# Kernel tuning notes

Hardware: AMD Instinct MI355X
Metric: run time of the kernel (lower is better)

## Reference

```python
import jax, jax.numpy as jnp
import numpy as np

EPS = 1e-5
HD = 16          # hidden_dim
OC = 256         # out_chs
NH = 8           # num_heads (groups of qkv conv)
DV = OC // (2 * HD)  # per-head value dim = 8


def conv_bn_silu(x, w, gamma, beta, mean, var, stride=1, pad=1, groups=1):
    # Conv2d(bias=False) + BatchNorm2d(eval) + SiLU, NCHW/OIHW
    y = jax.lax.conv_general_dilated(
        x, w, (stride, stride), [(pad, pad), (pad, pad)],
        dimension_numbers=('NCHW', 'OIHW', 'NCHW'),
        feature_group_count=groups)
    inv = gamma * jax.lax.rsqrt(var + EPS)
    y = y * inv[None, :, None, None] + (beta - mean * inv)[None, :, None, None]
    return y * jax.nn.sigmoid(y)


def _bn_params(key, c):
    k1, k2, k3, k4 = jax.random.split(key, 4)
    g = 1.0 + 0.1 * jax.random.normal(k1, (c,), jnp.float32)
    b = 0.1 * jax.random.normal(k2, (c,), jnp.float32)
    m = 0.1 * jax.random.normal(k3, (c,), jnp.float32)
    v = jax.random.uniform(k4, (c,), jnp.float32, 0.5, 1.5)
    return g, b, m, v


def setup_inputs() -> dict:
    key = jax.random.key(0)
    ks = jax.random.split(key, 8)
    B, C, H, W = 16, 256, 80, 80
    qkv_out = HD * 2 + OC // 2  # 160
    d = {}
    d['x'] = jax.random.normal(ks[0], (B, C, H, W), jnp.float32)
    # qkv_conv: grouped 3x3, groups=NH -> in per group = C//NH
    d['qkv_w'] = jax.random.normal(ks[1], (qkv_out, C // NH, 3, 3), jnp.float32) * 0.05
    d['qkv_g'], d['qkv_b'], d['qkv_m'], d['qkv_v'] = _bn_params(ks[2], qkv_out)
    # hidden_conv: dense 3x3
    d['hid_w'] = jax.random.normal(ks[3], (OC, C, 3, 3), jnp.float32) * 0.02
    d['hid_g'], d['hid_b'], d['hid_m'], d['hid_v'] = _bn_params(ks[4], OC)
    # out_conv: 1x1 on (OC//2*3) channels
    d['out_w'] = jax.random.normal(ks[5], (OC, OC // 2 * 3, 1, 1), jnp.float32) * 0.05
    d['out_g'], d['out_b'], d['out_m'], d['out_v'] = _bn_params(ks[6], OC)
    return d


def reference(x, qkv_w, qkv_g, qkv_b, qkv_m, qkv_v,
              hid_w, hid_g, hid_b, hid_m, hid_v,
              out_w, out_g, out_b, out_m, out_v):
    B, C, H, W = x.shape
    N = H * W
    qkv = conv_bn_silu(x, qkv_w, qkv_g, qkv_b, qkv_m, qkv_v, stride=1, pad=1, groups=NH)
    q = qkv[:, :HD]               # (B, HD, H, W)
    k = qkv[:, HD:2 * HD]
    v = qkv[:, 2 * HD:]           # (B, OC//2, H, W)
    # permute to (B, N, HD) / (B, N, HD, DV), channel-major reshape matches torch .view
    q = q.transpose(0, 2, 3, 1).reshape(B, N, HD)
    k = k.transpose(0, 2, 3, 1).reshape(B, N, HD)
    v = v.transpose(0, 2, 3, 1).reshape(B, N, HD, DV)
    # per-pixel tiny attention: attn[b,n,i,j] = softmax_j(q_i * k_j)
    attn = jax.nn.softmax(q[..., :, None] * k[..., None, :], axis=-1)  # (B,N,HD,HD)
    y = jnp.einsum('bnij,bnjd->bnid', attn, v)                          # (B,N,HD,DV)
    # torch: permute(0,2,3,1).view(B, OC//2, H, W)
    y = y.transpose(0, 2, 3, 1).reshape(B, OC // 2, H, W)
    h = conv_bn_silu(x, hid_w, hid_g, hid_b, hid_m, hid_v, stride=1, pad=1)
    y = jnp.concatenate([y, h], axis=1)  # (B, OC//2*3, H, W)
    return conv_bn_silu(y, out_w, out_g, out_b, out_m, out_v, stride=1, pad=0)
```

## Files before the change

kernel.cpp:

```cpp
#include <hip/hip_runtime.h>
#include <stdint.h>

typedef unsigned short u16;
typedef unsigned int u32;
typedef __attribute__((ext_vector_type(4))) float f32x4;
typedef __attribute__((ext_vector_type(8))) __bf16 bf16x8;

#define EPS_BN 1e-5f

__device__ __forceinline__ u16 f2bf(float f) {
  u32 u = __builtin_bit_cast(u32, f);
  u32 r = (u + 0x7fffu + ((u >> 16) & 1u)) >> 16;
  return (u16)r;
}

__device__ __forceinline__ float silu_f(float v) {
  return v / (1.0f + __expf(-v));
}

__device__ __forceinline__ void gll16(const void* g, void* l) {
  __builtin_amdgcn_global_load_lds(
      (__attribute__((address_space(1))) void*)(void*)g,
      (__attribute__((address_space(3))) void*)l, 16, 0, 0);
}

__global__ __launch_bounds__(256) void prep(
    const float* __restrict__ qkv_w, const float* __restrict__ qg,
    const float* __restrict__ qb, const float* __restrict__ qm,
    const float* __restrict__ qv,
    const float* __restrict__ hid_w, const float* __restrict__ hg,
    const float* __restrict__ hb, const float* __restrict__ hm,
    const float* __restrict__ hv,
    const float* __restrict__ out_w, const float* __restrict__ og,
    const float* __restrict__ ob, const float* __restrict__ om,
    const float* __restrict__ ov,
    u16* __restrict__ wtb, u16* __restrict__ w2b, u16* __restrict__ wqp,
    float* __restrict__ bnq_s, float* __restrict__ bnq_b,
    float* __restrict__ bnh_s, float* __restrict__ bnh_b,
    float* __restrict__ bn2s, float* __restrict__ bn2b,
    float* __restrict__ zpg)
{
  const int gid = blockIdx.x * 256 + threadIdx.x;
  if (gid < 256 * 2304) {
    int j = gid / 2304, k = gid - j * 2304;
    int tap = k >> 8, c = k & 255;
    wtb[gid] = f2bf(hid_w[(j * 256 + c) * 9 + tap]);
  }
  if (gid < 73728) {
    int g = gid / 9216;
    int r = gid - g * 9216;
    int j = r / 288, k = r - j * 288;
    int tap = k >> 5, cg = k & 31;
    float v = 0.f;
    if (j < 20) v = qkv_w[((g * 20 + j) * 32 + cg) * 9 + tap];
    wqp[gid] = f2bf(v);
  }
  if (gid < 98304) w2b[gid] = f2bf(out_w[gid]);
  if (gid < 160) {
    float iv = qg[gid] * rsqrtf(qv[gid] + EPS_BN);
    bnq_s[gid] = iv; bnq_b[gid] = qb[gid] - qm[gid] * iv;
  }
  if (gid < 256) {
    float iv = hg[gid] * rsqrtf(hv[gid] + EPS_BN);
    bnh_s[gid] = iv; bnh_b[gid] = hb[gid] - hm[gid] * iv;
    float iv2 = og[gid] * rsqrtf(ov[gid] + EPS_BN);
    bn2s[gid] = iv2; bn2b[gid] = ob[gid] - om[gid] * iv2;
  }
  if (gid < 64) zpg[gid] = 0.f;
}

__global__ __launch_bounds__(256) void nchw2nhwc(
    const float* __restrict__ x, u16* __restrict__ xn)
{
  __shared__ u16 T[80 * 66];
  const int t = threadIdx.x;
  const int ct = blockIdx.x;
  const int h  = blockIdx.y;
  const int b  = blockIdx.z;
  const float* src = x + ((size_t)b * 256 + ct * 64) * 6400 + h * 80;
  for (int it = 0; it < 5; ++it) {
    int idx = it * 256 + t;
    int cl = idx / 20, w4 = idx - cl * 20;
    float4 v = *(const float4*)(src + (size_t)cl * 6400 + w4 * 4);
    T[(w4 * 4 + 0) * 66 + cl] = f2bf(v.x);
    T[(w4 * 4 + 1) * 66 + cl] = f2bf(v.y);
    T[(w4 * 4 + 2) * 66 + cl] = f2bf(v.z);
    T[(w4 * 4 + 3) * 66 + cl] = f2bf(v.w);
  }
  __syncthreads();
  u16* dst = xn + ((size_t)(b * 80 + h) * 80) * 256 + ct * 64;
  for (int it = 0; it < 5; ++it) {
    int idx = it * 256 + t;
    int wl = idx >> 4;
    int cl = (idx & 15) * 4;
    ushort4 v4;
    v4.x = T[wl * 66 + cl + 0];
    v4.y = T[wl * 66 + cl + 1];
    v4.z = T[wl * 66 + cl + 2];
    v4.w = T[wl * 66 + cl + 3];
    *(ushort4*)(dst + (size_t)wl * 256 + cl) = v4;
  }
}

__global__ __launch_bounds__(512, 4) void gemm_main(
    const u16* __restrict__ xn, const u16* __restrict__ wt,
    const float* __restrict__ bns, const float* __restrict__ bnb,
    const float* __restrict__ zpg, u16* __restrict__ ycat)
{
  __shared__ __attribute__((aligned(16))) u16 Al[128 * 64];
  __shared__ __attribute__((aligned(16))) u16 Bl[256 * 64];
  const int t = threadIdx.x;
  const int wave = t >> 6, lane = t & 63;
  const int wm = wave >> 2;
  const int wn = wave & 3;
  const int orig = blockIdx.x;
  const int wg = (orig & 7) * 100 + (orig >> 3);
  const int ptile = wg * 128;

  const int srcc = (((lane & 7) ^ ((lane >> 3) & 7)) * 8);
  const int c16 = lane & 15, lq = lane >> 4;

  int pbA[2], hhA[2], wwA[2];
#pragma unroll
  for (int l = 0; l < 2; ++l) {
    int row = wave * 8 + (lane >> 3) + l * 64;
    int p = ptile + row;
    pbA[l] = p;
    int hw = p % 6400;
    hhA[l] = hw / 80;
    wwA[l] = hw - (hw / 80) * 80;
  }
  int bofB[4];
#pragma unroll
  for (int l = 0; l < 4; ++l) {
    int row = wave * 8 + (lane >> 3) + l * 64;
    bofB[l] = row * 2304 + srcc;
  }

  f32x4 acc[4][4];
#pragma unroll
  for (int m = 0; m < 4; ++m)
#pragma unroll
    for (int n = 0; n < 4; ++n) {
      f32x4 z = {0.f, 0.f, 0.f, 0.f};
      acc[m][n] = z;
    }

  for (int ks = 0; ks < 36; ++ks) {
    const int k0 = ks * 64;
    const int tap = ks >> 2;
    const int c0 = (ks & 3) * 64;
    const int dh = tap / 3 - 1, dw = tap - (tap / 3) * 3 - 1;
    const int dp = dh * 80 + dw;
    __syncthreads();
#pragma unroll
    for (int l = 0; l < 2; ++l) {
      bool ok = ((unsigned)(hhA[l] + dh) < 80u) & ((unsigned)(wwA[l] + dw) < 80u);
      const u16* src = ok
          ? (xn + ((size_t)(pbA[l] + dp) * 256 + c0 + srcc))
          : (const u16*)zpg;
      gll16(src, Al + (wave * 8 + l * 64) * 64);
    }
#pragma unroll
    for (int l = 0; l < 4; ++l)
      gll16(wt + (size_t)(bofB[l] + k0), Bl + (wave * 8 + l * 64) * 64);
    __syncthreads();
#pragma unroll
    for (int kk = 0; kk < 2; ++kk) {
      const int q = kk * 4 + lq;
      bf16x8 av[4], bv[4];
#pragma unroll
      for (int m = 0; m < 4; ++m) {
        int r = wm * 64 + m * 16 + c16;
        av[m] = *(const bf16x8*)(Al + r * 64 + (q ^ (r & 7)) * 8);
      }
#pragma unroll
      for (int n = 0; n < 4; ++n) {
        int j = wn * 64 + n * 16 + c16;
        bv[n] = *(const bf16x8*)(Bl + j * 64 + (q ^ (j & 7)) * 8);
      }
#pragma unroll
      for (int m = 0; m < 4; ++m)
#pragma unroll
        for (int n = 0; n < 4; ++n)
          acc[m][n] = __builtin_amdgcn_mfma_f32_16x16x32_bf16(
              av[m], bv[n], acc[m][n], 0, 0, 0);
    }
  }

  const int rg = lq;
#pragma unroll
  for (int n = 0; n < 4; ++n) {
    int j = wn * 64 + n * 16 + c16;
    float sc = bns[j], bi = bnb[j];
#pragma unroll
    for (int m = 0; m < 4; ++m) {
      int p0 = ptile + wm * 64 + m * 16 + rg * 4;
#pragma unroll
      for (int r = 0; r < 4; ++r) {
        float v = silu_f(acc[m][n][r] * sc + bi);
        ycat[(size_t)(p0 + r) * 384 + 128 + j] = f2bf(v);
      }
    }
  }
}

__global__ __launch_bounds__(256, 2) void qkv_attn(
    const u16* __restrict__ xn, const u16* __restrict__ wqp,
    const float* __restrict__ bnq_s, const float* __restrict__ bnq_b,
    u16* __restrict__ ycat)
{
  __shared__ __attribute__((aligned(16))) char LB[81920];
  u16* HB0 = (u16*)LB;
  u16* HB1 = (u16*)(LB + 40960);
  float* qs = (float*)LB;

  const int t = threadIdx.x;
  const int wave = t >> 6, lane = t & 63;
  const int orig = blockIdx.x;
  const int wg = (orig & 7) * 100 + (orig >> 3);
  const int ptile = wg * 128;
  const int pbase = ptile - 88;

  const int srcc = (((lane & 7) ^ ((lane >> 3) & 7)) * 8);
  const int q = lane >> 4, c16 = lane & 15;

  int ph[2], pw[2];
#pragma unroll
  for (int m = 0; m < 2; ++m) {
    int p = ptile + wave * 32 + m * 16 + c16;
    int hw = p % 6400;
    ph[m] = hw / 80;
    pw[m] = hw - (hw / 80) * 80;
  }

  auto STAGE_H = [&](int cc, u16* dst) {
#pragma unroll
    for (int r = 0; r < 10; ++r) {
      int row = r * 32 + wave * 8 + (lane >> 3);
      int p = pbase + row;
      int pc = p < 0 ? 0 : (p > 102399 ? 102399 : p);
      gll16(xn + (size_t)pc * 256 + cc * 64 + srcc,
            dst + (r * 32 + wave * 8) * 64);
    }
  };

  bf16x8 zv;
#pragma unroll
  for (int i = 0; i < 8; ++i) zv[i] = (__bf16)0.0f;

  f32x4 acc[2][16];
#pragma unroll
  for (int m = 0; m < 2; ++m)
#pragma unroll
    for (int f = 0; f < 16; ++f) {
      f32x4 z = {0.f, 0.f, 0.f, 0.f};
      acc[m][f] = z;
    }

  STAGE_H(0, HB0);
  asm volatile("s_waitcnt vmcnt(0)" ::: "memory");
  __builtin_amdgcn_sched_barrier(0);
  __syncthreads();

#pragma unroll
  for (int cc = 0; cc < 4; ++cc) {
    const u16* HBc = (cc & 1) ? HB1 : HB0;
    u16* HBn = (cc & 1) ? HB0 : HB1;
    if (cc < 3) STAGE_H(cc + 1, HBn);
    for (int tap = 0; tap < 9; ++tap) {
      const int dh = tap / 3 - 1, dw = tap - (tap / 3) * 3 - 1;
      const int dp = dh * 80 + dw;
      bf16x8 bq[2][2];
#pragma unroll
      for (int h = 0; h < 2; ++h)
#pragma unroll
        for (int nf = 0; nf < 2; ++nf) {
          int row = (2 * cc + h) * 32 + nf * 16 + c16;
          bq[h][nf] =
              *(const bf16x8*)(wqp + (size_t)row * 288 + tap * 32 + q * 8);
        }
      bf16x8 av[2][2];
#pragma unroll
      for (int m = 0; m < 2; ++m) {
        int rl = wave * 32 + m * 16 + c16 + 88 + dp;
        bool ok = ((unsigned)(ph[m] + dh) < 80u) &
                  ((unsigned)(pw[m] + dw) < 80u);
#pragma unroll
        for (int h = 0; h < 2; ++h) {
          int q8 = h * 4 + q;
          bf16x8 raw = *(const bf16x8*)(HBc + rl * 64 + ((q8 ^ (rl & 7)) * 8));
          av[m][h] = ok ? raw : zv;
        }
      }
#pragma unroll
      for (int h = 0; h < 2; ++h)
#pragma unroll
        for (int m = 0; m < 2; ++m)
#pragma unroll
          for (int nf = 0; nf < 2; ++nf)
            acc[m][(2 * cc + h) * 2 + nf] = __builtin_amdgcn_mfma_f32_16x16x32_bf16(
                av[m][h], bq[h][nf], acc[m][(2 * cc + h) * 2 + nf], 0, 0, 0);
    }
    if (cc < 3) {
      asm volatile("s_waitcnt vmcnt(0)" ::: "memory");
      __builtin_amdgcn_sched_barrier(0);
      __syncthreads();
    }
  }

  asm volatile("s_waitcnt vmcnt(0)" ::: "memory");
  __builtin_amdgcn_sched_barrier(0);
  __syncthreads();

#pragma unroll
  for (int f = 0; f < 16; ++f) {
    int jj = (f & 1) * 16 + c16;
    if (jj >= 20) continue;
    int oc = (f >> 1) * 20 + jj;
    float sc = bnq_s[oc], bi = bnq_b[oc];
#pragma unroll
    for (int m = 0; m < 2; ++m) {
      int pl0 = wave * 32 + m * 16 + q * 4;
#pragma unroll
      for (int r = 0; r < 4; ++r)
        qs[(pl0 + r) * 160 + oc] = silu_f(acc[m][f][r] * sc + bi);
    }
  }
  __syncthreads();

  for (int it = 0; it < 8; ++it) {
    int idx = it * 256 + t;
    int px = idx >> 4, i = idx & 15;
    const float* row = qs + px * 160;
    const float qi = row[i];
    float s[16];
    float mx = -3.4e38f;
#pragma unroll
    for (int j = 0; j < 16; ++j) { s[j] = qi * row[16 + j]; mx = fmaxf(mx, s[j]); }
    float sum = 0.f;
#pragma unroll
    for (int j = 0; j < 16; ++j) { s[j] = __expf(s[j] - mx); sum += s[j]; }
    const float inv = 1.0f / sum;
    float y[8];
#pragma unroll
    for (int d = 0; d < 8; ++d) y[d] = 0.f;
#pragma unroll
    for (int j = 0; j < 16; ++j) {
      const float a = s[j];
      const float* vr = row + 32 + j * 8;
#pragma unroll
      for (int d = 0; d < 8; ++d) y[d] += a * vr[d];
    }
    union { u16 u[8]; uint4 v4; } pk;
#pragma unroll
    for (int d = 0; d < 8; ++d) pk.u[d] = f2bf(y[d] * inv);
    *(uint4*)(ycat + (size_t)(ptile + px) * 384 + i * 8) = pk.v4;
  }
}

__global__ __launch_bounds__(256, 2) void gemm_out(
    const u16* __restrict__ w2, const u16* __restrict__ ycat,
    const float* __restrict__ bns, const float* __restrict__ bnb,
    float* __restrict__ out)
{
  __shared__ __attribute__((aligned(16))) u16 Al[128 * 64];
  __shared__ __attribute__((aligned(16))) u16 Bl[128 * 64];
  const int t = threadIdx.x;
  const int wave = t >> 6, lane = t & 63;
  const int wr = wave >> 1, wc = wave & 1;
  const int orig = blockIdx.y * 2 + blockIdx.x;
  const int wg = (orig & 7) * 200 + (orig >> 3);
  const int octile = (wg / 800) * 128;
  const int ptile = (wg % 800) * 128;

  const int srcc = (((lane & 7) ^ ((lane >> 3) & 7)) * 8);
  int bofA[4], bofB[4];
#pragma unroll
  for (int c = 0; c < 4; ++c) {
    int m = wave * 32 + c * 8 + (lane >> 3);
    bofA[c] = (octile + m) * 384 + srcc;
    bofB[c] = (ptile + m) * 384 + srcc;
  }
  u16* AlW = Al + wave * 2048;
  u16* BlW = Bl + wave * 2048;

  f32x4 acc[4][4];
#pragma unroll
  for (int m = 0; m < 4; ++m)
#pragma unroll
    for (int n = 0; n < 4; ++n) {
      f32x4 z = {0.f, 0.f, 0.f, 0.f};
      acc[m][n] = z;
    }

  for (int ks = 0; ks < 6; ++ks) {
    const int k0 = ks * 64;
    __syncthreads();
#pragma unroll
    for (int c = 0; c < 4; ++c) gll16(w2 + (size_t)(bofA[c] + k0), AlW + c * 512);
#pragma unroll
    for (int c = 0; c < 4; ++c) gll16(ycat + (size_t)(bofB[c] + k0), BlW + c * 512);
    __syncthreads();
#pragma unroll
    for (int kk = 0; kk < 2; ++kk) {
      const int q = kk * 4 + (lane >> 4);
      const int c16 = lane & 15;
      bf16x8 av[4], bv[4];
#pragma unroll
      for (int m = 0; m < 4; ++m) {
        int r = wr * 64 + m * 16 + c16;
        av[m] = *(const bf16x8*)(Al + r * 64 + (q ^ (r & 7)) * 8);
      }
#pragma unroll
      for (int n = 0; n < 4; ++n) {
        int r = wc * 64 + n * 16 + c16;
        bv[n] = *(const bf16x8*)(Bl + r * 64 + (q ^ (r & 7)) * 8);
      }
#pragma unroll
      for (int m = 0; m < 4; ++m)
#pragma unroll
        for (int n = 0; n < 4; ++n)
          acc[m][n] = __builtin_amdgcn_mfma_f32_16x16x32_bf16(
              av[m], bv[n], acc[m][n], 0, 0, 0);
    }
  }

  const int c16 = lane & 15, rg = lane >> 4;
  const int b = ptile / 6400;
  const int hwb = ptile - b * 6400;
#pragma unroll
  for (int m = 0; m < 4; ++m) {
    int oc0 = octile + wr * 64 + m * 16 + rg * 4;
#pragma unroll
    for (int n = 0; n < 4; ++n) {
      int hw = hwb + wc * 64 + n * 16 + c16;
#pragma unroll
      for (int r = 0; r < 4; ++r) {
        int oc = oc0 + r;
        float v = silu_f(acc[m][n][r] * bns[oc] + bnb[oc]);
        out[((size_t)b * 256 + oc) * 6400 + hw] = v;
      }
    }
  }
}

extern "C" void kernel_launch(void* const* d_in, const int* in_sizes, int n_in,
                              void* d_out, int out_size, void* d_ws, size_t ws_size,
                              hipStream_t stream) {
  (void)in_sizes; (void)n_in; (void)out_size; (void)ws_size;
  const float* x    = (const float*)d_in[0];
  const float* qkvw = (const float*)d_in[1];
  const float* qg   = (const float*)d_in[2];
  const float* qb   = (const float*)d_in[3];
  const float* qm   = (const float*)d_in[4];
  const float* qv   = (const float*)d_in[5];
  const float* hw_  = (const float*)d_in[6];
  const float* hg   = (const float*)d_in[7];
  const float* hb   = (const float*)d_in[8];
  const float* hm   = (const float*)d_in[9];
  const float* hv   = (const float*)d_in[10];
  const float* ow   = (const float*)d_in[11];
  const float* og   = (const float*)d_in[12];
  const float* ob   = (const float*)d_in[13];
  const float* om   = (const float*)d_in[14];
  const float* ov   = (const float*)d_in[15];

  char* ws = (char*)d_ws;
  float* zpg   = (float*)(ws + 0);
  float* bnq_s = (float*)(ws + 256);
  float* bnq_b = (float*)(ws + 1280);
  float* bnh_s = (float*)(ws + 2304);
  float* bnh_b = (float*)(ws + 3328);
  float* bn2s  = (float*)(ws + 4352);
  float* bn2b  = (float*)(ws + 5376);
  u16*   wtb   = (u16*)(ws + 6400);
  u16*   w2b   = (u16*)(ws + 1186048);
  u16*   wqp   = (u16*)(ws + 1382656);
  u16*   xn    = (u16*)(ws + 1536000);
  u16*   ycat  = (u16*)(ws + 119500800);
  float* out   = (float*)d_out;

  prep<<<dim3(2304), dim3(256), 0, stream>>>(
      qkvw, qg, qb, qm, qv, hw_, hg, hb, hm, hv, ow, og, ob, om, ov,
      wtb, w2b, wqp, bnq_s, bnq_b, bnh_s, bnh_b, bn2s, bn2b, zpg);
  nchw2nhwc<<<dim3(4, 80, 16), dim3(256), 0, stream>>>(x, xn);
  gemm_main<<<dim3(800), dim3(512), 0, stream>>>(
      xn, wtb, bnh_s, bnh_b, zpg, ycat);
  qkv_attn<<<dim3(800), dim3(256), 0, stream>>>(
      xn, wqp, bnq_s, bnq_b, ycat);
  gemm_out<<<dim3(2, 800), dim3(256), 0, stream>>>(
      w2b, ycat, bn2s, bn2b, out);
}
```

Before: 302.4 us.

## Load input halo once per channel chunk and reuse across all 3x3 taps

The implicit-GEMM 3x3 conv now loads a 320-row halo of input pixels per 64-channel chunk into LDS once and reads shifted rows for each of the 9 taps, instead of reloading the A tile for every tap. Out-of-image taps are masked in registers with a zero vector, so the zero-page global pointer is no longer needed. This is meant to cut global/L2 traffic for the activation operand roughly ninefold. In exchange LDS use grows (320x64 A plus 256x64 B per block), which can reduce occupancy, and the swizzled reads at shifted rows may introduce bank conflicts.

```diff
diff --git a/kernel.cpp b/kernel.cpp
--- a/kernel.cpp
+++ b/kernel.cpp
@@ -105,9 +105,9 @@
 __global__ __launch_bounds__(512, 4) void gemm_main(
     const u16* __restrict__ xn, const u16* __restrict__ wt,
     const float* __restrict__ bns, const float* __restrict__ bnb,
-    const float* __restrict__ zpg, u16* __restrict__ ycat)
+    u16* __restrict__ ycat)
 {
-  __shared__ __attribute__((aligned(16))) u16 Al[128 * 64];
+  __shared__ __attribute__((aligned(16))) u16 HA[320 * 64];
   __shared__ __attribute__((aligned(16))) u16 Bl[256 * 64];
   const int t = threadIdx.x;
   const int wave = t >> 6, lane = t & 63;
@@ -116,26 +116,29 @@
   const int orig = blockIdx.x;
   const int wg = (orig & 7) * 100 + (orig >> 3);
   const int ptile = wg * 128;
+  const int pbase = ptile - 88;
 
   const int srcc = (((lane & 7) ^ ((lane >> 3) & 7)) * 8);
   const int c16 = lane & 15, lq = lane >> 4;
 
-  int pbA[2], hhA[2], wwA[2];
-#pragma unroll
-  for (int l = 0; l < 2; ++l) {
-    int row = wave * 8 + (lane >> 3) + l * 64;
-    int p = ptile + row;
-    pbA[l] = p;
+  int ph[4], pw[4];
+#pragma unroll
+  for (int m = 0; m < 4; ++m) {
+    int p = ptile + wm * 64 + m * 16 + c16;
     int hw = p % 6400;
-    hhA[l] = hw / 80;
-    wwA[l] = hw - (hw / 80) * 80;
+    ph[m] = hw / 80;
+    pw[m] = hw - (hw / 80) * 80;
   }
   int bofB[4];
 #pragma unroll
   for (int l = 0; l < 4; ++l) {
-    int row = wave * 8 + (lane >> 3) + l * 64;
+    int row = l * 64 + wave * 8 + (lane >> 3);
     bofB[l] = row * 2304 + srcc;
   }
+
+  bf16x8 zv;
+#pragma unroll
+  for (int i = 0; i < 8; ++i) zv[i] = (__bf16)0.0f;
 
   f32x4 acc[4][4];
 #pragma unroll
@@ -146,45 +149,52 @@
       acc[m][n] = z;
     }
 
-  for (int ks = 0; ks < 36; ++ks) {
-    const int k0 = ks * 64;
-    const int tap = ks >> 2;
-    const int c0 = (ks & 3) * 64;
-    const int dh = tap / 3 - 1, dw = tap - (tap / 3) * 3 - 1;
-    const int dp = dh * 80 + dw;
+#pragma unroll
+  for (int cc = 0; cc < 4; ++cc) {
+    const int c0 = cc * 64;
     __syncthreads();
 #pragma unroll
-    for (int l = 0; l < 2; ++l) {
-      bool ok = ((unsigned)(hhA[l] + dh) < 80u) & ((unsigned)(wwA[l] + dw) < 80u);
-      const u16* src = ok
-          ? (xn + ((size_t)(pbA[l] + dp) * 256 + c0 + srcc))
-          : (const u16*)zpg;
-      gll16(src, Al + (wave * 8 + l * 64) * 64);
-    }
-#pragma unroll
-    for (int l = 0; l < 4; ++l)
-      gll16(wt + (size_t)(bofB[l] + k0), Bl + (wave * 8 + l * 64) * 64);
-    __syncthreads();
-#pragma unroll
-    for (int kk = 0; kk < 2; ++kk) {
-      const int q = kk * 4 + lq;
-      bf16x8 av[4], bv[4];
-#pragma unroll
-      for (int m = 0; m < 4; ++m) {
-        int r = wm * 64 + m * 16 + c16;
-        av[m] = *(const bf16x8*)(Al + r * 64 + (q ^ (r & 7)) * 8);
+    for (int r = 0; r < 5; ++r) {
+      int row = r * 64 + wave * 8 + (lane >> 3);
+      int p = pbase + row;
+      int pc = p < 0 ? 0 : (p > 102399 ? 102399 : p);
+      gll16(xn + (size_t)pc * 256 + c0 + srcc, HA + (r * 64 + wave * 8) * 64);
+    }
+    for (int tap = 0; tap < 9; ++tap) {
+      const int dh = tap / 3 - 1, dw = tap - (tap / 3) * 3 - 1;
+      const int dp = dh * 80 + dw;
+      const int k0 = tap * 256 + c0;
+      __syncthreads();
+#pragma unroll
+      for (int l = 0; l < 4; ++l)
+        gll16(wt + (size_t)(bofB[l] + k0), Bl + (l * 64 + wave * 8) * 64);
+      __syncthreads();
+      bool ok[4];
+#pragma unroll
+      for (int m = 0; m < 4; ++m)
+        ok[m] = ((unsigned)(ph[m] + dh) < 80u) & ((unsigned)(pw[m] + dw) < 80u);
+#pragma unroll
+      for (int kk = 0; kk < 2; ++kk) {
+        const int q = kk * 4 + lq;
+        bf16x8 av[4], bv[4];
+#pragma unroll
+        for (int m = 0; m < 4; ++m) {
+          int rl = wm * 64 + m * 16 + c16 + 88 + dp;
+          bf16x8 raw = *(const bf16x8*)(HA + rl * 64 + (q ^ (rl & 7)) * 8);
+          av[m] = ok[m] ? raw : zv;
+        }
+#pragma unroll
+        for (int n = 0; n < 4; ++n) {
+          int j = wn * 64 + n * 16 + c16;
+          bv[n] = *(const bf16x8*)(Bl + j * 64 + (q ^ (j & 7)) * 8);
+        }
+#pragma unroll
+        for (int m = 0; m < 4; ++m)
+#pragma unroll
+          for (int n = 0; n < 4; ++n)
+            acc[m][n] = __builtin_amdgcn_mfma_f32_16x16x32_bf16(
+                av[m], bv[n], acc[m][n], 0, 0, 0);
       }
-#pragma unroll
-      for (int n = 0; n < 4; ++n) {
-        int j = wn * 64 + n * 16 + c16;
-        bv[n] = *(const bf16x8*)(Bl + j * 64 + (q ^ (j & 7)) * 8);
-      }
-#pragma unroll
-      for (int m = 0; m < 4; ++m)
-#pragma unroll
-        for (int n = 0; n < 4; ++n)
-          acc[m][n] = __builtin_amdgcn_mfma_f32_16x16x32_bf16(
-              av[m], bv[n], acc[m][n], 0, 0, 0);
     }
   }
 
@@ -486,7 +496,7 @@
       wtb, w2b, wqp, bnq_s, bnq_b, bnh_s, bnh_b, bn2s, bn2b, zpg);
   nchw2nhwc<<<dim3(4, 80, 16), dim3(256), 0, stream>>>(x, xn);
   gemm_main<<<dim3(800), dim3(512), 0, stream>>>(
-      xn, wtb, bnh_s, bnh_b, zpg, ycat);
+      xn, wtb, bnh_s, bnh_b, ycat);
   qkv_attn<<<dim3(800), dim3(256), 0, stream>>>(
       xn, wqp, bnq_s, bnq_b, ycat);
   gemm_out<<<dim3(2, 800), dim3(256), 0, stream>>>(
```

Result: slower. 343.2 us (+13.5%).
